# Kernel tuning notes

Measured on AMD Instinct MI355X. Metric: run time of the kernel, lower is better.

Reference implementation:

```python
import jax, jax.numpy as jnp
import numpy as np

DIM = 1536
NH = 12
HD = DIM // NH          # 128
C = HD // 2             # 64 rotary pairs
F, H, W = 6, 20, 20
L = F * H * W           # 2400
B = 1
MAX_POS = 1024
EPS = 1e-6


def _rope_freqs():
    """[MAX_POS, C, 2, 2] rotation matrices, split [22,21,21] across f/h/w axes."""
    c0 = C - 2 * (C // 3)           # 22
    c1 = C // 3                      # 21
    pos = np.arange(MAX_POS, dtype=np.float32)
    parts = []
    for m in (c0, c1, c1):
        inv = 1.0 / (10000.0 ** (np.arange(m, dtype=np.float32) / m))
        parts.append(pos[:, None] * inv[None, :])
    ang = np.concatenate(parts, axis=1)          # [MAX_POS, C]
    cos, sin = np.cos(ang), np.sin(ang)
    # R[..., j, k]: rows [cos, -sin], [sin, cos]
    R = np.stack([np.stack([cos, -sin], -1), np.stack([sin, cos], -1)], -2)
    return jnp.asarray(R, dtype=jnp.float32)


def setup_inputs() -> dict:
    key = jax.random.key(0)
    ks = jax.random.split(key, 12)
    s = 1.0 / np.sqrt(DIM)
    lin = lambda k: (jax.random.normal(k, (DIM, DIM), jnp.float32) * s)
    return {
        "x": jax.random.normal(ks[0], (B, L, DIM), jnp.float32),
        "Wq": lin(ks[1]), "bq": jax.random.normal(ks[2], (DIM,), jnp.float32) * 0.01,
        "Wk": lin(ks[3]), "bk": jax.random.normal(ks[4], (DIM,), jnp.float32) * 0.01,
        "Wv": lin(ks[5]), "bv": jax.random.normal(ks[6], (DIM,), jnp.float32) * 0.01,
        "Wo": lin(ks[7]), "bo": jax.random.normal(ks[8], (DIM,), jnp.float32) * 0.01,
        "gq": jnp.ones((DIM,), jnp.float32),
        "gk": jnp.ones((DIM,), jnp.float32),
        "seq_lens": jnp.full((B,), L, dtype=jnp.int32),
        "grid_sizes": jnp.asarray([[F, H, W]], dtype=jnp.int32),
        "freqs": _rope_freqs(),
    }


def _rms_norm(x, g, eps=EPS):
    # WanRMSNorm: x * rsqrt(mean(x^2, -1) + eps) * weight
    return x * jax.lax.rsqrt(jnp.mean(jnp.square(x), axis=-1, keepdims=True) + eps) * g


def _rope_apply(xh, grid_sizes, freqs):
    """xh: [B, L, n, d]; freqs: [MAX_POS, c, 2, 2]. All samples share one grid."""
    b, l, n, d = xh.shape
    c = d // 2
    c0 = c - 2 * (c // 3)
    c1 = c // 3
    f, h, w = (int(v) for v in np.asarray(grid_sizes[0]))
    # build per-position 3D rotation matrices: [f*h*w, c, 2, 2]
    fa = jnp.broadcast_to(freqs[:f, :c0][:, None, None], (f, h, w, c0, 2, 2))
    fb = jnp.broadcast_to(freqs[:h, c0:c0 + c1][None, :, None], (f, h, w, c1, 2, 2))
    fc = jnp.broadcast_to(freqs[:w, c0 + c1:c][None, None, :], (f, h, w, c1, 2, 2))
    R = jnp.concatenate([fa, fb, fc], axis=3).reshape(f * h * w, c, 2, 2)
    xp = xh.reshape(b, l, n, c, 2)
    out = jnp.einsum('lcjk,blnck->blncj', R, xp)
    return out.reshape(b, l, n, d)


def reference(x, Wq, bq, Wk, bk, Wv, bv, Wo, bo, gq, gk, seq_lens, grid_sizes, freqs):
    b, l = x.shape[:2]
    q = _rms_norm(x @ Wq.T + bq, gq).reshape(b, l, NH, HD)
    k = _rms_norm(x @ Wk.T + bk, gk).reshape(b, l, NH, HD)
    v = (x @ Wv.T + bv).reshape(b, l, NH, HD)
    q = _rope_apply(q, grid_sizes, freqs)
    k = _rope_apply(k, grid_sizes, freqs)
    # full attention with key-length mask (window_size=(-1,-1))
    scores = jnp.einsum('bqnd,bknd->bnqk', q, k) / np.sqrt(HD)
    kmask = jnp.arange(l)[None, :] < seq_lens[:, None]          # [B, L]
    scores = jnp.where(kmask[:, None, None, :], scores, -1e9)
    attn = jax.nn.softmax(scores, axis=-1)
    out = jnp.einsum('bnqk,bknd->bqnd', attn, v).reshape(b, l, DIM)
    return out @ Wo.T + bo
```

## Files before the change

### kernel.cpp

```cpp
#include <hip/hip_runtime.h>
#include <hip/hip_bf16.h>
#include <stdint.h>


#define DIM  1536
#define NH   12
#define HD   128
#define LSEQ 2400
#define LPAD 2432
#define KT2  32
#define NT2  (LPAD / KT2)
#define NTQ  19

typedef __attribute__((ext_vector_type(8))) short short8;
typedef __attribute__((ext_vector_type(8))) _Float16 half8;
typedef __attribute__((ext_vector_type(4))) float f32x4;
typedef unsigned short ushort_t;
typedef unsigned int   uint32;

__device__ __forceinline__ ushort_t f2bf(float f) {
  union { float f; unsigned u; } v; v.f = f;
  unsigned r = (v.u + 0x7fffu + ((v.u >> 16) & 1u)) >> 16;
  return (ushort_t)r;
}
__device__ __forceinline__ float bf2f(ushort_t h) {
  union { unsigned u; float f; } v; v.u = ((unsigned)h) << 16;
  return v.f;
}
__device__ __forceinline__ void async16(void* lds, const void* g) {
  __builtin_amdgcn_global_load_lds(
      (const __attribute__((address_space(1))) uint32*)g,
      (__attribute__((address_space(3))) uint32*)lds, 16, 0, 0);
}
__device__ __forceinline__ uint4 pack8(const float* f) {
  uint4 u;
  u.x = (uint32)f2bf(f[0]) | ((uint32)f2bf(f[1]) << 16);
  u.y = (uint32)f2bf(f[2]) | ((uint32)f2bf(f[3]) << 16);
  u.z = (uint32)f2bf(f[4]) | ((uint32)f2bf(f[5]) << 16);
  u.w = (uint32)f2bf(f[6]) | ((uint32)f2bf(f[7]) << 16);
  return u;
}

__global__ void cvt_all(const float* __restrict__ x,
                        const float* __restrict__ W0, const float* __restrict__ W1,
                        const float* __restrict__ W2, const float* __restrict__ W3,
                        ushort_t* __restrict__ xd,
                        ushort_t* __restrict__ d0, ushort_t* __restrict__ d1,
                        ushort_t* __restrict__ d2, ushort_t* __restrict__ d3)
{
  const int z = blockIdx.y;
  const int i = blockIdx.x * 256 + threadIdx.x;
  if (z == 0) {
    uint4 u = {0, 0, 0, 0};
    if (i * 8 < LSEQ * DIM) {
      float f[8];
      *(float4*)f = *(const float4*)(x + i * 8);
      *(float4*)(f + 4) = *(const float4*)(x + i * 8 + 4);
      u = pack8(f);
    }
    *(uint4*)(xd + i * 8) = u;
    return;
  }
  if (blockIdx.x >= DIM * DIM / 2048) return;
  const float* s = (z == 1) ? W0 : ((z == 2) ? W1 : ((z == 3) ? W2 : W3));
  ushort_t* d    = (z == 1) ? d0 : ((z == 2) ? d1 : ((z == 3) ? d2 : d3));
  float f[8];
  *(float4*)f = *(const float4*)(s + i * 8);
  *(float4*)(f + 4) = *(const float4*)(s + i * 8 + 4);
  *(uint4*)(d + i * 8) = pack8(f);
}

template<int OUT_F32>
__global__ __launch_bounds__(256) void gemm_bt(
    const ushort_t* __restrict__ Ap,
    const ushort_t* __restrict__ B0, const ushort_t* __restrict__ B1, const ushort_t* __restrict__ B2,
    const float* __restrict__ b0, const float* __restrict__ b1, const float* __restrict__ b2,
    void* __restrict__ D0, void* __restrict__ D1, void* __restrict__ D2,
    int Mout)
{
  const int z = blockIdx.y;
  const ushort_t* Bw  = (z == 0) ? B0 : ((z == 1) ? B1 : B2);
  const float* bias   = (z == 0) ? b0 : ((z == 1) ? b1 : b2);
  void* D             = (z == 0) ? D0 : ((z == 1) ? D1 : D2);

  const int bm = blockIdx.x / 12, bn = blockIdx.x % 12;
  const int tid = threadIdx.x;
  const int w = tid >> 6, lam = tid & 63;
  const int wr = w >> 1, wc = w & 1;
  const int lane15 = lam & 15, quad = lam >> 4;

  __shared__ __align__(16) char lds[32768];
  char* sA = lds;
  char* sB = lds + 16384;

  f32x4 acc[4][4];
#pragma unroll
  for (int i = 0; i < 4; ++i)
#pragma unroll
    for (int j = 0; j < 4; ++j) acc[i][j] = {};

  const int sm = (w * 32) + (lam >> 3);
  const int sc = (lam & 7);

  for (int k0 = 0; k0 < DIM; k0 += 64) {
    __syncthreads();
#pragma unroll
    for (int i = 0; i < 4; ++i) {
      const int li = w * 4096 + i * 1024;
      const int m = sm + i * 8;
      const int c = sc ^ (m & 7);
      async16(sA + li, Ap + (size_t)(bm * 128 + m) * DIM + k0 + c * 8);
      async16(sB + li, Bw + (size_t)(bn * 128 + m) * DIM + k0 + c * 8);
    }
    __syncthreads();
#pragma unroll
    for (int kc = 0; kc < 2; ++kc) {
      const int chunk = kc * 4 + quad;
      short8 af[4], bfr[4];
#pragma unroll
      for (int i = 0; i < 4; ++i) {
        const int m = wr * 64 + i * 16 + lane15;
        af[i] = *(const short8*)(sA + m * 128 + ((chunk ^ (m & 7)) * 16));
      }
#pragma unroll
      for (int j = 0; j < 4; ++j) {
        const int n = wc * 64 + j * 16 + lane15;
        bfr[j] = *(const short8*)(sB + n * 128 + ((chunk ^ (n & 7)) * 16));
      }
#pragma unroll
      for (int i = 0; i < 4; ++i)
#pragma unroll
        for (int j = 0; j < 4; ++j)
          acc[i][j] = __builtin_amdgcn_mfma_f32_16x16x32_bf16(af[i], bfr[j], acc[i][j], 0, 0, 0);
    }
  }

#pragma unroll
  for (int j = 0; j < 4; ++j) {
    const int n = bn * 128 + wc * 64 + j * 16 + lane15;
    const float bv = bias[n];
#pragma unroll
    for (int i = 0; i < 4; ++i) {
      const int mb = bm * 128 + wr * 64 + i * 16 + quad * 4;
#pragma unroll
      for (int r = 0; r < 4; ++r) {
        const int m = mb + r;
        const float val = acc[i][j][r] + bv;
        if (OUT_F32) {
          if (m < Mout) ((float*)D)[(size_t)m * DIM + n] = val;
        } else {
          ((ushort_t*)D)[(size_t)m * DIM + n] = f2bf(val);
        }
      }
    }
  }
}

__global__ __launch_bounds__(256) void nr_vp(
    const ushort_t* __restrict__ qpre, const ushort_t* __restrict__ kpre,
    const ushort_t* __restrict__ vbf,
    const float* __restrict__ gq, const float* __restrict__ gk,
    const float* __restrict__ freqs,
    const int* __restrict__ seq_lens, const int* __restrict__ grid_sizes,
    ushort_t* __restrict__ qh, ushort_t* __restrict__ kh,
    ushort_t* __restrict__ vp)
{
  const int bx = blockIdx.x;
  const int tid = threadIdx.x;
  __shared__ float wsum[4];
  __shared__ float srstd;
  __shared__ ushort_t tbuf[32][33];

  if (bx >= 2 * LPAD) {
    const int vb = bx - 2 * LPAD;
    const int head = vb / (NT2 * 4);
    const int rem = vb - head * (NT2 * 4);
    const int t2 = rem >> 2;
    const int d0 = (rem & 3) * 32;
    const int l0 = t2 * 32;
    const int tx = tid & 31, ty = tid >> 5;
#pragma unroll
    for (int rr = 0; rr < 4; ++rr)
      tbuf[ty * 4 + rr][tx] = vbf[(size_t)(l0 + ty * 4 + rr) * DIM + head * HD + d0 + tx];
    __syncthreads();
#pragma unroll
    for (int rr = 0; rr < 4; ++rr) {
      const int d = d0 + ty * 4 + rr;
      vp[(((size_t)head * NT2 + t2) * HD + d) * KT2 + tx] = tbuf[tx][ty * 4 + rr];
    }
    return;
  }

  const int row = bx >> 1;
  const int which = bx & 1;
  const ushort_t* src = which ? kpre : qpre;
  const float* g = which ? gk : gq;
  ushort_t* dst = which ? kh : qh;

  float s = 0.f;
  if (tid < 192) {
    uint4 u = *(const uint4*)(src + (size_t)row * DIM + tid * 8);
    const uint32 uu[4] = {u.x, u.y, u.z, u.w};
#pragma unroll
    for (int i = 0; i < 4; ++i) {
      float a = bf2f((ushort_t)(uu[i] & 0xffff));
      float b = bf2f((ushort_t)(uu[i] >> 16));
      s += a * a + b * b;
    }
  }
#pragma unroll
  for (int off = 32; off; off >>= 1) s += __shfl_down(s, off, 64);
  if ((tid & 63) == 0) wsum[tid >> 6] = s;
  __syncthreads();
  if (tid == 0)
    srstd = rsqrtf((wsum[0] + wsum[1] + wsum[2] + wsum[3]) / (float)DIM + 1e-6f);
  __syncthreads();
  const float rstd = srstd;

  const int seq = seq_lens[0];
  const int h_ = grid_sizes[1], w_ = grid_sizes[2];
  const int hw = h_ * w_;
  const int fidx = row / hw;
  const int rem = row - fidx * hw;
  const int hidx = rem / w_;
  const int widx = rem - hidx * w_;
  const bool live = row < seq;

#pragma unroll
  for (int pp = 0; pp < 3; ++pp) {
    const int p = tid + pp * 256;
    const int c = p & 63, head = p >> 6;
    const int e_in = head * HD + 2 * c;
    uint32 xin = *(const uint32*)(src + (size_t)row * DIM + e_in);
    float x0 = bf2f((ushort_t)(xin & 0xffff));
    float x1 = bf2f((ushort_t)(xin >> 16));
    float2 gg = *(const float2*)(g + e_in);
    float y0 = x0 * rstd * gg.x, y1 = x1 * rstd * gg.y;
    const int pos = (c < 22) ? fidx : ((c < 43) ? hidx : widx);
    float4 R = *(const float4*)(freqs + ((size_t)pos * 64 + c) * 4);
    float o0 = R.x * y0 + R.y * y1;
    float o1 = R.z * y0 + R.w * y1;
    uint32 op = live ? ((uint32)f2bf(o0) | ((uint32)f2bf(o1) << 16)) : 0u;
    *(uint32*)(dst + ((size_t)head * LPAD + row) * HD + 2 * c) = op;
  }
}

__global__ __launch_bounds__(256, 3) void attn7(
    const ushort_t* __restrict__ qh, const ushort_t* __restrict__ kh,
    const ushort_t* __restrict__ vp, const int* __restrict__ seq_lens,
    _Float16* __restrict__ op0, _Float16* __restrict__ op1,
    _Float16* __restrict__ op2, _Float16* __restrict__ op3,
    float* __restrict__ lp)
{
  const int qz = blockIdx.z;
  const int head = blockIdx.y;
  const int q0 = blockIdx.x * 128;
  const int tid = threadIdx.x;
  const int w = tid >> 6, lam = tid & 63;
  const int lane15 = lam & 15, quad = lam >> 4;
  const int seq = seq_lens[0];
  _Float16* op = (qz == 0) ? op0 : ((qz == 1) ? op1 : ((qz == 2) ? op2 : op3));

  __shared__ __align__(16) char kbuf[2][8192];
  __shared__ __align__(16) char vbuf[2][8192];
  __shared__ __align__(16) ushort_t pbuf[4][32][32];

  const ushort_t* qbase = qh + ((size_t)head * LPAD + q0 + w * 32) * HD;
  short8 qf[2][4];
#pragma unroll
  for (int qt = 0; qt < 2; ++qt)
#pragma unroll
    for (int kc = 0; kc < 4; ++kc)
      qf[qt][kc] = *(const short8*)(qbase + (qt * 16 + lane15) * HD + kc * 32 + quad * 8);

  f32x4 o[2][8];
#pragma unroll
  for (int qt = 0; qt < 2; ++qt)
#pragma unroll
    for (int dt = 0; dt < 8; ++dt) o[qt][dt] = {};
  float lacc[2][4] = {};

  const float c1 = 0.12751744510848893f;
  const float c2 = 17.312340490667562f;

  const ushort_t* khh = kh + (size_t)head * LPAD * HD;
  const ushort_t* vph = vp + (size_t)head * NT2 * HD * KT2;

  const int krow0 = w * 8 + (lam >> 4);
  const int kslot = lam & 15;

#define STAGE(gt, b)                                                     \
  {                                                                      \
    const ushort_t* kg = khh + (size_t)(gt) * (KT2 * HD);                \
    const ushort_t* vg = vph + (size_t)(gt) * (HD * KT2);                \
    _Pragma("unroll")                                                    \
    for (int i = 0; i < 2; ++i) {                                        \
      const int li = w * 2048 + i * 1024;                                \
      const int kr = krow0 + i * 4;                                      \
      const int kc_ = kslot ^ (kr & 15);                                 \
      async16(kbuf[b] + li, kg + kr * HD + kc_ * 8);                     \
      const int G = w * 128 + i * 64 + lam;                              \
      const int l_ = (G >> 2) & 15;                                      \
      const int cc = (G & 3) ^ (l_ & 3);                                 \
      const int d_ = ((G >> 6) << 4) + l_;                               \
      async16(vbuf[b] + li, vg + d_ * KT2 + cc * 8);                     \
    }                                                                    \
  }

  const int tbase = qz * NTQ;
  STAGE(tbase, 0)
  __syncthreads();

  for (int t = 0; t < NTQ; ++t) {
    const int b = t & 1;
    const int gt = tbase + t;
    if (t + 1 < NTQ) STAGE(gt + 1, b ^ 1)

    f32x4 S[2][2];
    S[0][0] = {}; S[0][1] = {}; S[1][0] = {}; S[1][1] = {};
#pragma unroll
    for (int n0 = 0; n0 < 2; ++n0)
#pragma unroll
      for (int kc = 0; kc < 4; ++kc) {
        short8 kf = *(const short8*)(kbuf[b] + (n0 * 16 + lane15) * 256 +
                                     (((kc * 4 + quad) ^ lane15) * 16));
#pragma unroll
        for (int qt = 0; qt < 2; ++qt)
          S[qt][n0] = __builtin_amdgcn_mfma_f32_16x16x32_bf16(qf[qt][kc], kf, S[qt][n0], 0, 0, 0);
      }

#pragma unroll
    for (int n0 = 0; n0 < 2; ++n0) {
      const bool valid = (gt * KT2 + n0 * 16 + lane15) < seq;
#pragma unroll
      for (int qt = 0; qt < 2; ++qt)
#pragma unroll
        for (int r = 0; r < 4; ++r) {
          float e = valid ? exp2f(S[qt][n0][r] * c1 - c2) : 0.f;
          lacc[qt][r] += e;
          const int prow = qt * 16 + quad * 4 + r;
          const int pcol = n0 * 16 + lane15;
          pbuf[w][prow][(((pcol >> 3) ^ ((prow >> 2) & 3)) << 3) | (pcol & 7)] = f2bf(e);
        }
    }
    asm volatile("s_waitcnt lgkmcnt(0)" ::: "memory");

    short8 pf[2];
#pragma unroll
    for (int qt = 0; qt < 2; ++qt)
      pf[qt] = *(const short8*)(&pbuf[w][qt * 16 + lane15][(quad ^ ((lane15 >> 2) & 3)) << 3]);
#pragma unroll
    for (int dt = 0; dt < 8; ++dt) {
      short8 vf = *(const short8*)(vbuf[b] + dt * 1024 +
                                   (lane15 * 4 + (quad ^ (lane15 & 3))) * 16);
#pragma unroll
      for (int qt = 0; qt < 2; ++qt)
        o[qt][dt] = __builtin_amdgcn_mfma_f32_16x16x32_bf16(pf[qt], vf, o[qt][dt], 0, 0, 0);
    }
    __syncthreads();
  }
#undef STAGE

#pragma unroll
  for (int qt = 0; qt < 2; ++qt) {
    float lrow[4], linv[4];
#pragma unroll
    for (int r = 0; r < 4; ++r) {
      float l = lacc[qt][r];
#pragma unroll
      for (int off = 1; off < 16; off <<= 1) l += __shfl_xor(l, off, 16);
      lrow[r] = l;
      linv[r] = 1.0f / l;
    }
    if (lane15 == 0) {
#pragma unroll
      for (int r = 0; r < 4; ++r)
        lp[((size_t)qz * NH + head) * LPAD + q0 + w * 32 + qt * 16 + quad * 4 + r] = lrow[r];
    }
#pragma unroll
    for (int dt = 0; dt < 8; ++dt)
#pragma unroll
      for (int r = 0; r < 4; ++r) {
        const int m = q0 + w * 32 + qt * 16 + quad * 4 + r;
        op[(size_t)m * DIM + head * HD + dt * 16 + lane15] =
            (_Float16)(o[qt][dt][r] * linv[r]);
      }
  }
}

__global__ void merge(const _Float16* __restrict__ o0, const _Float16* __restrict__ o1,
                      const _Float16* __restrict__ o2, const _Float16* __restrict__ o3,
                      const float* __restrict__ lp, ushort_t* __restrict__ attno)
{
  const int i = blockIdx.x * 256 + threadIdx.x;
  const int e = i * 8;
  const int m = e / DIM;
  const int head = (e - m * DIM) >> 7;
  float l[4];
#pragma unroll
  for (int h = 0; h < 4; ++h) l[h] = lp[((size_t)h * NH + head) * LPAD + m];
  const float inv = 1.0f / (l[0] + l[1] + l[2] + l[3]);
  half8 a = *(const half8*)(o0 + e);
  half8 b = *(const half8*)(o1 + e);
  half8 c = *(const half8*)(o2 + e);
  half8 d = *(const half8*)(o3 + e);
  const float w0 = l[0] * inv, w1 = l[1] * inv, w2 = l[2] * inv, w3 = l[3] * inv;
  float f[8];
#pragma unroll
  for (int j = 0; j < 8; ++j)
    f[j] = (float)a[j] * w0 + (float)b[j] * w1 + (float)c[j] * w2 + (float)d[j] * w3;
  *(uint4*)(attno + e) = pack8(f);
}

extern "C" void kernel_launch(void* const* d_in, const int* in_sizes, int n_in,
                              void* d_out, int out_size, void* d_ws, size_t ws_size,
                              hipStream_t stream)
{
  const float* x  = (const float*)d_in[0];
  const float* Wq = (const float*)d_in[1];
  const float* bq = (const float*)d_in[2];
  const float* Wk = (const float*)d_in[3];
  const float* bk = (const float*)d_in[4];
  const float* Wv = (const float*)d_in[5];
  const float* bv = (const float*)d_in[6];
  const float* Wo = (const float*)d_in[7];
  const float* bo = (const float*)d_in[8];
  const float* gq = (const float*)d_in[9];
  const float* gk = (const float*)d_in[10];
  const int* seq_lens   = (const int*)d_in[11];
  const int* grid_sizes = (const int*)d_in[12];
  const float* freqs    = (const float*)d_in[13];
  float* out = (float*)d_out;

  const size_t BUF = (size_t)LPAD * DIM * 2;
  const size_t WB  = (size_t)DIM * DIM * 2;
  char* ws = (char*)d_ws;
  dim3 blk(256);

  ushort_t* xbf  = (ushort_t*)(ws);
  ushort_t* wqb  = (ushort_t*)(ws + BUF);
  ushort_t* wkb  = (ushort_t*)(ws + BUF + WB);
  ushort_t* wvb  = (ushort_t*)(ws + BUF + 2 * WB);
  ushort_t* wob  = (ushort_t*)(ws + BUF + 3 * WB);
  ushort_t* qpre = (ushort_t*)(ws + BUF + 4 * WB);
  ushort_t* kpre = (ushort_t*)(ws + 2 * BUF + 4 * WB);
  ushort_t* qh   = (ushort_t*)(ws + 3 * BUF + 4 * WB);
  ushort_t* kh   = (ushort_t*)(ws + 4 * BUF + 4 * WB);
  ushort_t* vbf  = (ushort_t*)(ws + 5 * BUF + 4 * WB);
  ushort_t* vp    = xbf;
  ushort_t* attno = xbf;
  _Float16* op0 = (_Float16*)qpre;
  _Float16* op1 = (_Float16*)kpre;
  _Float16* op2 = (_Float16*)vbf;
  _Float16* op3 = (_Float16*)wqb;
  float*    lp  = (float*)wvb;

  cvt_all<<<dim3(LPAD * DIM / 2048, 5), blk, 0, stream>>>(
      x, Wq, Wk, Wv, Wo, xbf, wqb, wkb, wvb, wob);
  gemm_bt<0><<<dim3(228, 3), blk, 0, stream>>>(
      xbf, wqb, wkb, wvb, bq, bk, bv, qpre, kpre, vbf, 0);
  nr_vp<<<dim3(2 * LPAD + NH * NT2 * 4), blk, 0, stream>>>(
      qpre, kpre, vbf, gq, gk, freqs, seq_lens, grid_sizes, qh, kh, vp);
  attn7<<<dim3(LPAD / 128, NH, 4), blk, 0, stream>>>(
      qh, kh, vp, seq_lens, op0, op1, op2, op3, lp);
  merge<<<dim3(LPAD * DIM / 2048), blk, 0, stream>>>(op0, op1, op2, op3, lp, attno);
  gemm_bt<1><<<dim3(228, 1), blk, 0, stream>>>(
      attno, wob, wob, wob, bo, bo, bo, out, out, out, LSEQ);
}
```

Measured before the change: 300.8 us.

## Compute transposed S so P stays in registers, dropping LDS round-trip

After: 293.9 us. -2.3%, faster.

```diff
diff --git a/kernel.cpp b/kernel.cpp
--- a/kernel.cpp
+++ b/kernel.cpp
@@ -183,10 +183,11 @@
     for (int rr = 0; rr < 4; ++rr)
       tbuf[ty * 4 + rr][tx] = vbf[(size_t)(l0 + ty * 4 + rr) * DIM + head * HD + d0 + tx];
     __syncthreads();
+    const int tx2 = ((tx >> 2) & 3) * 8 + (tx >> 4) * 4 + (tx & 3);
 #pragma unroll
     for (int rr = 0; rr < 4; ++rr) {
       const int d = d0 + ty * 4 + rr;
-      vp[(((size_t)head * NT2 + t2) * HD + d) * KT2 + tx] = tbuf[tx][ty * 4 + rr];
+      vp[(((size_t)head * NT2 + t2) * HD + d) * KT2 + tx2] = tbuf[tx][ty * 4 + rr];
     }
     return;
   }
@@ -245,7 +246,7 @@
   }
 }
 
-__global__ __launch_bounds__(256, 3) void attn7(
+__global__ __launch_bounds__(256, 3) void attn8(
     const ushort_t* __restrict__ qh, const ushort_t* __restrict__ kh,
     const ushort_t* __restrict__ vp, const int* __restrict__ seq_lens,
     _Float16* __restrict__ op0, _Float16* __restrict__ op1,
@@ -263,7 +264,6 @@
 
   __shared__ __align__(16) char kbuf[2][8192];
   __shared__ __align__(16) char vbuf[2][8192];
-  __shared__ __align__(16) ushort_t pbuf[4][32][32];
 
   const ushort_t* qbase = qh + ((size_t)head * LPAD + q0 + w * 32) * HD;
   short8 qf[2][4];
@@ -278,7 +278,7 @@
   for (int qt = 0; qt < 2; ++qt)
 #pragma unroll
     for (int dt = 0; dt < 8; ++dt) o[qt][dt] = {};
-  float lacc[2][4] = {};
+  float lacc[2] = {};
 
   const float c1 = 0.12751744510848893f;
   const float c2 = 17.312340490667562f;
@@ -300,10 +300,8 @@
       const int kc_ = kslot ^ (kr & 15);                                 \
       async16(kbuf[b] + li, kg + kr * HD + kc_ * 8);                     \
       const int G = w * 128 + i * 64 + lam;                              \
-      const int l_ = (G >> 2) & 15;                                      \
-      const int cc = (G & 3) ^ (l_ & 3);                                 \
-      const int d_ = ((G >> 6) << 4) + l_;                               \
-      async16(vbuf[b] + li, vg + d_ * KT2 + cc * 8);                     \
+      const int vdt = G >> 6, vdd = (G >> 2) & 15, vqq = G & 3;          \
+      async16(vbuf[b] + li, vg + (vdt * 16 + vdd) * KT2 + vqq * 8);      \
     }                                                                    \
   }
 
@@ -326,36 +324,38 @@
                                      (((kc * 4 + quad) ^ lane15) * 16));
 #pragma unroll
         for (int qt = 0; qt < 2; ++qt)
-          S[qt][n0] = __builtin_amdgcn_mfma_f32_16x16x32_bf16(qf[qt][kc], kf, S[qt][n0], 0, 0, 0);
-      }
-
-#pragma unroll
-    for (int n0 = 0; n0 < 2; ++n0) {
-      const bool valid = (gt * KT2 + n0 * 16 + lane15) < seq;
+          S[qt][n0] = __builtin_amdgcn_mfma_f32_16x16x32_bf16(kf, qf[qt][kc], S[qt][n0], 0, 0, 0);
+      }
+
+    short8 pa8[2];
+#pragma unroll
+    for (int qt = 0; qt < 2; ++qt) {
+      float ev[8];
+      float s8 = 0.f;
+#pragma unroll
+      for (int n0 = 0; n0 < 2; ++n0) {
+        const int kb0 = gt * KT2 + n0 * 16 + quad * 4;
+#pragma unroll
+        for (int r = 0; r < 4; ++r) {
+          float e = (kb0 + r < seq) ? exp2f(S[qt][n0][r] * c1 - c2) : 0.f;
+          ev[n0 * 4 + r] = e;
+          s8 += e;
+        }
+      }
+      lacc[qt] += s8;
+      union { uint32 u[4]; short8 s; } pk;
+#pragma unroll
+      for (int p = 0; p < 4; ++p)
+        pk.u[p] = (uint32)f2bf(ev[2 * p]) | ((uint32)f2bf(ev[2 * p + 1]) << 16);
+      pa8[qt] = pk.s;
+    }
+
+#pragma unroll
+    for (int dt = 0; dt < 8; ++dt) {
+      short8 vf = *(const short8*)(vbuf[b] + dt * 1024 + lane15 * 64 + quad * 16);
 #pragma unroll
       for (int qt = 0; qt < 2; ++qt)
-#pragma unroll
-        for (int r = 0; r < 4; ++r) {
-          float e = valid ? exp2f(S[qt][n0][r] * c1 - c2) : 0.f;
-          lacc[qt][r] += e;
-          const int prow = qt * 16 + quad * 4 + r;
-          const int pcol = n0 * 16 + lane15;
-          pbuf[w][prow][(((pcol >> 3) ^ ((prow >> 2) & 3)) << 3) | (pcol & 7)] = f2bf(e);
-        }
-    }
-    asm volatile("s_waitcnt lgkmcnt(0)" ::: "memory");
-
-    short8 pf[2];
-#pragma unroll
-    for (int qt = 0; qt < 2; ++qt)
-      pf[qt] = *(const short8*)(&pbuf[w][qt * 16 + lane15][(quad ^ ((lane15 >> 2) & 3)) << 3]);
-#pragma unroll
-    for (int dt = 0; dt < 8; ++dt) {
-      short8 vf = *(const short8*)(vbuf[b] + dt * 1024 +
-                                   (lane15 * 4 + (quad ^ (lane15 & 3))) * 16);
-#pragma unroll
-      for (int qt = 0; qt < 2; ++qt)
-        o[qt][dt] = __builtin_amdgcn_mfma_f32_16x16x32_bf16(pf[qt], vf, o[qt][dt], 0, 0, 0);
+        o[qt][dt] = __builtin_amdgcn_mfma_f32_16x16x32_bf16(pa8[qt], vf, o[qt][dt], 0, 0, 0);
     }
     __syncthreads();
   }
@@ -363,20 +363,15 @@
 
 #pragma unroll
   for (int qt = 0; qt < 2; ++qt) {
-    float lrow[4], linv[4];
-#pragma unroll
-    for (int r = 0; r < 4; ++r) {
-      float l = lacc[qt][r];
-#pragma unroll
-      for (int off = 1; off < 16; off <<= 1) l += __shfl_xor(l, off, 16);
-      lrow[r] = l;
-      linv[r] = 1.0f / l;
-    }
-    if (lane15 == 0) {
-#pragma unroll
-      for (int r = 0; r < 4; ++r)
-        lp[((size_t)qz * NH + head) * LPAD + q0 + w * 32 + qt * 16 + quad * 4 + r] = lrow[r];
-    }
+    float l = lacc[qt];
+    l += __shfl_xor(l, 16, 64);
+    l += __shfl_xor(l, 32, 64);
+    if (lam < 16)
+      lp[((size_t)qz * NH + head) * LPAD + q0 + w * 32 + qt * 16 + lam] = l;
+    const float lrcp = 1.0f / l;
+    float linv[4];
+#pragma unroll
+    for (int r = 0; r < 4; ++r) linv[r] = __shfl(lrcp, quad * 4 + r, 64);
 #pragma unroll
     for (int dt = 0; dt < 8; ++dt)
 #pragma unroll
@@ -461,7 +456,7 @@
       xbf, wqb, wkb, wvb, bq, bk, bv, qpre, kpre, vbf, 0);
   nr_vp<<<dim3(2 * LPAD + NH * NT2 * 4), blk, 0, stream>>>(
       qpre, kpre, vbf, gq, gk, freqs, seq_lens, grid_sizes, qh, kh, vp);
-  attn7<<<dim3(LPAD / 128, NH, 4), blk, 0, stream>>>(
+  attn8<<<dim3(LPAD / 128, NH, 4), blk, 0, stream>>>(
       qh, kh, vp, seq_lens, op0, op1, op2, op3, lp);
   merge<<<dim3(LPAD * DIM / 2048), blk, 0, stream>>>(op0, op1, op2, op3, lp, attno);
   gemm_bt<1><<<dim3(228, 1), blk, 0, stream>>>(
```
